# Kernel optimization log

Hardware: AMD Instinct MI355X
Metric: run time of the kernel (lower is better)

Reference implementation:

```python
import jax, jax.numpy as jnp
import numpy as np

B, T, V, Dw, Df, H, L, F_ = 16, 96, 32000, 512, 512, 1024, 100, 64
EPS = 1e-8
SOS = 0


def setup_inputs() -> dict:
    key = jax.random.key(0)
    ks = jax.random.split(key, 24)
    rn = lambda k, s, sc=0.02: (jax.random.normal(k, s) * sc).astype(jnp.float32)
    pos_mask = (jax.random.uniform(ks[1], (B, F_, L)) < 0.3).astype(jnp.float32)
    pos_mask = jnp.maximum(pos_mask, jax.nn.one_hot(jnp.zeros((B, F_), jnp.int32), L))
    return {
        "fact_embeddings": rn(ks[0], (B, F_, Df), 1.0),
        "pos_mask": pos_mask,
        "emb": rn(ks[2], (V, Dw), 0.05),
        "W_ih": rn(ks[3], (4 * H, Df + Dw + L)),
        "W_hh": rn(ks[4], (4 * H, H)),
        "b_ih": jnp.zeros(4 * H, jnp.float32),
        "b_hh": jnp.zeros(4 * H, jnp.float32),
        "Wf1": rn(ks[5], (H, H + Df)), "bf1": jnp.zeros(H, jnp.float32),
        "Wf2": rn(ks[6], (Df, H)), "bf2": jnp.zeros(Df, jnp.float32),
        "Wc1": rn(ks[7], (H, H + Df)), "bc1": jnp.zeros(H, jnp.float32),
        "Wc2": rn(ks[8], (1, H)), "bc2": jnp.zeros(1, jnp.float32),
        "Wv1": rn(ks[9], (H, H + Df)), "bv1": jnp.zeros(H, jnp.float32),
        "Wv2": rn(ks[10], (Dw, H)), "bv2": jnp.zeros(Dw, jnp.float32),
        "Wp1": rn(ks[11], (H, H + Df)), "bp1": jnp.zeros(H, jnp.float32),
        "Wp2": rn(ks[12], (100, H)), "bp2": jnp.zeros(100, jnp.float32),
        "WP": rn(ks[13], (L, 100)), "bP": jnp.zeros(L, jnp.float32),
        "true_w": jax.random.randint(ks[14], (B, T), 0, L),
        "true_a": jax.random.randint(ks[15], (B, T), 0, F_),
        "true_z": jax.random.randint(ks[16], (B, T), 0, 2),
        "num_facts": jax.random.randint(ks[17], (B,), 1, F_),
    }


def reference(fact_embeddings, pos_mask, emb, W_ih, W_hh, b_ih, b_hh,
              Wf1, bf1, Wf2, bf2, Wc1, bc1, Wc2, bc2,
              Wv1, bv1, Wv2, bv2, Wp1, bp1, Wp2, bp2, WP, bP,
              true_w, true_a, true_z, num_facts):
    def mlp(x, W1, b1, W2, b2):
        return W2 @ jax.nn.relu(W1 @ x + b1) + b2

    def single(fe, pmask_b, tw, ta, tz, nf):
        # fe: [F_, Df]  pmask_b: [F_, L]  tw/ta/tz: [T]
        idx = jnp.arange(F_)
        valid = (idx < nf).astype(jnp.float32)
        attn_mask = jnp.where(idx == F_ - 1, 1.0, valid)  # NaF slot always allowed
        e_k = (fe * valid[:, None]).sum(0) / nf.astype(jnp.float32)

        def step(carry, inputs):
            a_prev, h, c, wv, wo = carry
            w_t, a_true, z_true = inputs
            x = jnp.concatenate([a_prev, wv, wo])  # [Df+Dw+L]
            gates = W_ih @ x + b_ih + W_hh @ h + b_hh
            i_g, f_g, g_g, o_g = jnp.split(gates, 4)
            c = jax.nn.sigmoid(f_g) * c + jax.nn.sigmoid(i_g) * jnp.tanh(g_g)
            h = jax.nn.sigmoid(o_g) * jnp.tanh(c)
            oe = jnp.concatenate([h, e_k])
            k_fact = mlp(oe, Wf1, bf1, Wf2, bf2)           # [Df]
            prob_a = jax.nn.softmax(fe @ k_fact)           # [F_]
            m = attn_mask * prob_a + EPS
            m = m / m.sum()
            log_m = jnp.log(m)
            a_idx = jnp.argmax(m)
            a_vec = fe[a_idx]
            oa = jnp.concatenate([h, a_vec])
            z = jax.nn.sigmoid(mlp(oa, Wc1, bc1, Wc2, bc2))[0]
            k_voca = mlp(oa, Wv1, bv1, Wv2, bv2)           # [Dw]
            log_w = jax.nn.log_softmax(emb @ k_voca)       # [V]
            k_pos = mlp(oa, Wp1, bp1, Wp2, bp2)            # [100]
            prob_pos = jax.nn.softmax(WP @ k_pos + bP)     # [L]
            mp = pmask_b[a_true] * prob_pos + EPS
            mp = mp / mp.sum()
            log_pos = jnp.log(mp)
            zf = z_true.astype(jnp.float32)
            loss = (-log_m[a_true]
                    + jnp.where(z_true == 0, -log_w[w_t], -log_pos[w_t])
                    - (zf * jnp.log(z) + (1.0 - zf) * jnp.log(1.0 - z)))
            wv_next = jnp.where(z_true == 0, emb[w_t], jnp.zeros(Dw, jnp.float32))
            wo_next = jnp.where(z_true == 0, jnp.zeros(L, jnp.float32), jax.nn.one_hot(w_t, L))
            return (a_vec, h, c, wv_next, wo_next), loss

        carry0 = (jnp.zeros(Df, jnp.float32), jnp.zeros(H, jnp.float32),
                  jnp.zeros(H, jnp.float32), emb[SOS], jnp.zeros(L, jnp.float32))
        _, losses = jax.lax.scan(step, carry0, (tw, ta, tz))
        return losses.sum()

    return jax.vmap(single)(fact_embeddings, pos_mask, true_w, true_a, true_z, num_facts).sum()
```

## Files before the change

kernel.cpp:

```cpp
#include <hip/hip_runtime.h>
#include <math.h>

#define TT 96
#define VV 32000
#define EPSF 1e-8f

typedef __attribute__((ext_vector_type(8))) short short8;
typedef __attribute__((ext_vector_type(4))) float f4v;

__device__ __forceinline__ float wsum64(float v){
  #pragma unroll
  for (int m=32;m>0;m>>=1) v += __shfl_xor(v,m);
  return v;
}
__device__ __forceinline__ float sigm(float x){ return 1.0f/(1.0f+expf(-x)); }
__device__ __forceinline__ float softplus(float x){ return x>20.0f ? x : log1pf(expf(x)); }
__device__ __forceinline__ float bf2f(unsigned short u){ return __uint_as_float(((unsigned)u)<<16); }
__device__ __forceinline__ unsigned short f2bf(float f){
  unsigned u = __float_as_uint(f);
  return (unsigned short)((u + 0x7fffu + ((u>>16)&1u)) >> 16);
}

__device__ __forceinline__ void core_chunk(
  const float4* __restrict__ w0, const float4* __restrict__ w1,
  const float4* __restrict__ w2, const float4* __restrict__ w3,
  const float4* __restrict__ xl, int l, int g, float (&acc)[4][4])
{
  #pragma unroll
  for (int kt=0; kt<8; kt++){
    int i = kt*16 + l;
    float4 a0=w0[i], a1=w1[i], a2=w2[i], a3=w3[i];
    #pragma unroll
    for (int j=0;j<4;j++){
      float4 x = xl[(4*g+j)*129 + i];
      acc[0][j] += a0.x*x.x + a0.y*x.y + a0.z*x.z + a0.w*x.w;
      acc[1][j] += a1.x*x.x + a1.y*x.y + a1.z*x.z + a1.w*x.w;
      acc[2][j] += a2.x*x.x + a2.y*x.y + a2.z*x.z + a2.w*x.w;
      acc[3][j] += a3.x*x.x + a3.y*x.y + a3.z*x.z + a3.w*x.w;
    }
  }
}

__device__ __forceinline__ float reduce_pick(float (&acc)[4][4], int l){
  float r = 0.f;
  #pragma unroll
  for (int ri=0;ri<4;ri++)
  #pragma unroll
  for (int j=0;j<4;j++){
    float v = acc[ri][j];
    v += __shfl_xor(v,1); v += __shfl_xor(v,2);
    v += __shfl_xor(v,4); v += __shfl_xor(v,8);
    if (l == ri*4+j) r = v;
  }
  return r;
}


__global__ __launch_bounds__(256) void k_step1(
  const float* __restrict__ Whh, float* __restrict__ hall,
  const float* __restrict__ Pw, const float* __restrict__ Pa,
  const int* __restrict__ aall, float* __restrict__ c, int t)
{
  __shared__ float4 xl[16*129];
  __shared__ float sg[256];
  int tid = threadIdx.x, lane = tid & 63, wave = tid >> 6;
  int l = lane & 15, g = lane >> 4;
  int j0 = blockIdx.x*4;
  const float4* h4 = (const float4*)hall + (size_t)t*4096;
  float acc[4][4] = {};
  for (int kc=0; kc<2; kc++){
    for (int idx=tid; idx<2048; idx+=256){
      int b = idx>>7, i = idx&127;
      xl[b*129+i] = h4[b*256 + kc*128 + i];
    }
    __syncthreads();
    const float4* w0 = (const float4*)(Whh + (size_t)(wave*1024 + j0+0)*1024) + kc*128;
    const float4* w1 = (const float4*)(Whh + (size_t)(wave*1024 + j0+1)*1024) + kc*128;
    const float4* w2 = (const float4*)(Whh + (size_t)(wave*1024 + j0+2)*1024) + kc*128;
    const float4* w3 = (const float4*)(Whh + (size_t)(wave*1024 + j0+3)*1024) + kc*128;
    core_chunk(w0,w1,w2,w3, xl, l, g, acc);
    __syncthreads();
  }
  float v = reduce_pick(acc, l);
  int r = l>>2;
  int b = g*4 + (l&3);
  int row = wave*1024 + j0 + r;
  float e = Pw[((size_t)(b*96+t))*4096 + row];
  if (t > 0){
    int ai = aall[(t-1)*16 + b];
    e += Pa[((size_t)(b*64+ai))*4096 + row];
  }
  sg[wave*64 + r*16 + b] = v + e;
  __syncthreads();
  if (tid < 64){
    int jj = j0 + (tid>>4), bb = tid&15;
    float ig = sg[  0 + (tid>>4)*16 + bb];
    float fg = sg[ 64 + (tid>>4)*16 + bb];
    float gg = sg[128 + (tid>>4)*16 + bb];
    float og = sg[192 + (tid>>4)*16 + bb];
    int ci = bb*1024 + jj;
    float cn = sigm(fg)*c[ci] + sigm(ig)*tanhf(gg);
    c[ci] = cn;
    hall[((size_t)(t+1)*16 + bb)*1024 + jj] = sigm(og)*tanhf(cn);
  }
}

__global__ __launch_bounds__(256) void k_tf(
  const float* __restrict__ Wf1, const float* __restrict__ hall,
  const float* __restrict__ cf, float* __restrict__ tf, int t)
{
  __shared__ float4 xl[16*129];
  int tid = threadIdx.x, lane = tid & 63, wave = tid >> 6;
  int l = lane & 15, g = lane >> 4;
  int rl0 = blockIdx.x*16 + wave*4;
  const float4* h4 = (const float4*)hall + (size_t)(t+1)*4096;
  float acc[4][4] = {};
  for (int kc=0; kc<2; kc++){
    for (int idx=tid; idx<2048; idx+=256){
      int b = idx>>7, i = idx&127;
      xl[b*129+i] = h4[b*256 + kc*128 + i];
    }
    __syncthreads();
    const float4* w0 = (const float4*)(Wf1 + (size_t)(rl0+0)*1536) + kc*128;
    const float4* w1 = (const float4*)(Wf1 + (size_t)(rl0+1)*1536) + kc*128;
    const float4* w2 = (const float4*)(Wf1 + (size_t)(rl0+2)*1536) + kc*128;
    const float4* w3 = (const float4*)(Wf1 + (size_t)(rl0+3)*1536) + kc*128;
    core_chunk(w0,w1,w2,w3, xl, l, g, acc);
    __syncthreads();
  }
  float v = reduce_pick(acc, l);
  int rl = rl0 + (l>>2);
  int b = g*4 + (l&3);
  tf[b*1024 + rl] = fmaxf(v + cf[b*1024 + rl], 0.f);
}

__global__ __launch_bounds__(256) void k_fk(
  const float* __restrict__ Wf2, const float* __restrict__ bf2,
  const float* __restrict__ tf, float* __restrict__ kfact)
{
  __shared__ float4 xl[16*129];
  int tid = threadIdx.x, lane = tid & 63, wave = tid >> 6;
  int l = lane & 15, g = lane >> 4;
  int row0 = blockIdx.x*16 + wave*4;
  const float4* X4 = (const float4*)tf;
  float acc[4][4] = {};
  for (int kc=0; kc<2; kc++){
    for (int idx=tid; idx<2048; idx+=256){
      int b = idx>>7, i = idx&127;
      xl[b*129+i] = X4[b*256 + kc*128 + i];
    }
    __syncthreads();
    const float4* w0 = (const float4*)(Wf2 + (size_t)(row0+0)*1024) + kc*128;
    const float4* w1 = (const float4*)(Wf2 + (size_t)(row0+1)*1024) + kc*128;
    const float4* w2 = (const float4*)(Wf2 + (size_t)(row0+2)*1024) + kc*128;
    const float4* w3 = (const float4*)(Wf2 + (size_t)(row0+3)*1024) + kc*128;
    core_chunk(w0,w1,w2,w3, xl, l, g, acc);
    __syncthreads();
  }
  float v = reduce_pick(acc, l);
  int row = row0 + (l>>2);
  int b = g*4 + (l&3);
  kfact[b*512 + row] = v + bf2[row];
}

__global__ __launch_bounds__(256) void k_attn(
  const float* __restrict__ fe, const float* __restrict__ kfact,
  const int* __restrict__ ta, const int* __restrict__ nfp,
  int* __restrict__ aall, float* __restrict__ loss, int t)
{
  __shared__ float sS[64];
  int b = blockIdx.x, tid = threadIdx.x;
  int f = tid >> 2, q = tid & 3;
  const float4* fe4 = (const float4*)(fe + ((size_t)b*64 + f)*512);
  const float4* kf4 = (const float4*)(kfact + b*512);
  float acc = 0.f;
  for (int j=0;j<32;j++){
    int i = q*32 + j;
    float4 a = fe4[i], k = kf4[i];
    acc += a.x*k.x + a.y*k.y + a.z*k.z + a.w*k.w;
  }
  acc += __shfl_xor(acc,1);
  acc += __shfl_xor(acc,2);
  if (q==0) sS[f] = acc;
  __syncthreads();
  if (tid < 64){
    int nf = nfp[b];
    float s = sS[tid];
    float mx = s;
    #pragma unroll
    for (int m=32;m>0;m>>=1) mx = fmaxf(mx, __shfl_xor(mx,m));
    float p = expf(s - mx);
    float ps = wsum64(p);
    p /= ps;
    bool mask = (tid < nf) || (tid == 63);
    float mval = mask ? (p + EPSF) : EPSF;
    float msum = wsum64(mval);
    float bv = mval; int bi2 = tid;
    #pragma unroll
    for (int m=32;m>0;m>>=1){
      float ov = __shfl_xor(bv,m); int oi = __shfl_xor(bi2,m);
      if (ov > bv || (ov == bv && oi < bi2)){ bv = ov; bi2 = oi; }
    }
    int at = ta[b*TT + t];
    float mat = __shfl(mval, at);
    if (tid == 0){
      atomicAdd(loss, -(logf(mat) - logf(msum)));
      aall[t*16 + b] = bi2;
    }
  }
}


__global__ __launch_bounds__(256) void k2_cvp(
  const float* __restrict__ Wc1, const float* __restrict__ Wv1,
  const float* __restrict__ Wp1, const float* __restrict__ hall,
  const float* __restrict__ Ph, const int* __restrict__ aall,
  const float* __restrict__ bc1, const float* __restrict__ bv1,
  const float* __restrict__ bp1, float* __restrict__ tcvp)
{
  __shared__ float4 xl[16*129];
  int tid = threadIdx.x, lane = tid & 63, wave = tid >> 6;
  int l = lane & 15, g = lane >> 4;
  int seg = blockIdx.x >> 6;
  int rl0 = (blockIdx.x & 63)*16 + wave*4;
  const float* W = (seg==0)?Wc1:(seg==1)?Wv1:Wp1;
  const float4* h4 = (const float4*)hall + (size_t)(16 + blockIdx.y*16)*256;
  float acc[4][4] = {};
  for (int kc=0; kc<2; kc++){
    for (int idx=tid; idx<2048; idx+=256){
      int cc = idx>>7, i = idx&127;
      xl[cc*129+i] = h4[cc*256 + kc*128 + i];
    }
    __syncthreads();
    const float4* w0 = (const float4*)(W + (size_t)(rl0+0)*1536) + kc*128;
    const float4* w1 = (const float4*)(W + (size_t)(rl0+1)*1536) + kc*128;
    const float4* w2 = (const float4*)(W + (size_t)(rl0+2)*1536) + kc*128;
    const float4* w3 = (const float4*)(W + (size_t)(rl0+3)*1536) + kc*128;
    core_chunk(w0,w1,w2,w3, xl, l, g, acc);
    __syncthreads();
  }
  float v = reduce_pick(acc, l);
  int rl = rl0 + (l>>2);
  int n = blockIdx.y*16 + g*4 + (l&3);
  int b = n & 15;
  int ai = aall[n];
  const float* bias = (seg==0)?bc1:(seg==1)?bv1:bp1;
  float vv = v + Ph[((size_t)(b*64+ai))*3072 + seg*1024 + rl] + bias[rl];
  tcvp[(size_t)n*3072 + seg*1024 + rl] = fmaxf(vv, 0.f);
}

__global__ __launch_bounds__(256) void k2_heads2(
  const float* __restrict__ Wv2, const float* __restrict__ bv2,
  const float* __restrict__ Wp2, const float* __restrict__ bp2,
  const float* __restrict__ Wc2, const float* __restrict__ bc2,
  const float* __restrict__ tcvp, unsigned short* __restrict__ kvh,
  float* __restrict__ kpall, float* __restrict__ zlall)
{
  __shared__ float4 xl[16*129];
  int tid = threadIdx.x, lane = tid & 63, wave = tid >> 6;
  int l = lane & 15, g = lane >> 4;
  int bx = blockIdx.x;
  int seg = (bx < 32) ? 0 : (bx < 39) ? 1 : 2;
  int rb  = (seg==0) ? bx*16 : (seg==1) ? (bx-32)*16 : 0;
  int rl0 = rb + wave*4;
  const float* WS = (seg==0)?Wv2:(seg==1)?Wp2:Wc2;
  int maxr = (seg==0)?511:(seg==1)?99:0;
  int xoff4 = (seg==0)?256:(seg==1)?512:0;
  const float4* X4 = (const float4*)tcvp;
  float acc[4][4] = {};
  for (int kc=0; kc<2; kc++){
    for (int idx=tid; idx<2048; idx+=256){
      int cc = idx>>7, i = idx&127;
      xl[cc*129+i] = X4[(size_t)(blockIdx.y*16+cc)*768 + xoff4 + kc*128 + i];
    }
    __syncthreads();
    const float4* w0 = (const float4*)(WS + (size_t)min(rl0+0,maxr)*1024) + kc*128;
    const float4* w1 = (const float4*)(WS + (size_t)min(rl0+1,maxr)*1024) + kc*128;
    const float4* w2 = (const float4*)(WS + (size_t)min(rl0+2,maxr)*1024) + kc*128;
    const float4* w3 = (const float4*)(WS + (size_t)min(rl0+3,maxr)*1024) + kc*128;
    core_chunk(w0,w1,w2,w3, xl, l, g, acc);
    __syncthreads();
  }
  float v = reduce_pick(acc, l);
  int rl = rl0 + (l>>2);
  int n = blockIdx.y*16 + g*4 + (l&3);
  if (seg==0) kvh[(size_t)n*512 + rl] = f2bf(v + bv2[rl]);
  else if (seg==1){ if (rl < 100) kpall[n*128 + rl] = v + bp2[rl]; }
  else { if (rl == 0) zlall[n] = v + bc2[0]; }
}

__global__ __launch_bounds__(256) void k2_vocab(
  const unsigned short* __restrict__ embh, const unsigned short* __restrict__ kvh,
  float2* __restrict__ part)
{
  int wid = blockIdx.x*4 + (threadIdx.x>>6);
  int lane = threadIdx.x & 63;
  int mtile = wid % 500, ntile = wid / 500;
  int mrow = mtile*64 + (lane&15);
  int ncol = ntile*64 + (lane&15);
  int ko = (lane>>4)*8;
  f4v acc[4][4];
  #pragma unroll
  for (int i=0;i<4;i++)
  #pragma unroll
  for (int j=0;j<4;j++)
  #pragma unroll
  for (int r=0;r<4;r++) acc[i][j][r] = 0.f;
  for (int kk=0; kk<512; kk+=32){
    short8 af[4], bfr[4];
    #pragma unroll
    for (int i=0;i<4;i++)
      af[i] = *(const short8*)(embh + (size_t)(mrow+16*i)*512 + kk + ko);
    #pragma unroll
    for (int i=0;i<4;i++)
      bfr[i] = *(const short8*)(kvh + (size_t)(ncol+16*i)*512 + kk + ko);
    #pragma unroll
    for (int i=0;i<4;i++)
      #pragma unroll
      for (int j=0;j<4;j++)
        acc[i][j] = __builtin_amdgcn_mfma_f32_16x16x32_bf16(af[i], bfr[j], acc[i][j], 0,0,0);
  }
  int q = lane>>4;
  #pragma unroll
  for (int j=0;j<4;j++){
    float mx = -3.4e38f;
    #pragma unroll
    for (int i=0;i<4;i++)
    #pragma unroll
    for (int r=0;r<4;r++) mx = fmaxf(mx, acc[i][j][r]);
    mx = fmaxf(mx, __shfl_xor(mx,16));
    mx = fmaxf(mx, __shfl_xor(mx,32));
    float s = 0.f;
    #pragma unroll
    for (int i=0;i<4;i++)
    #pragma unroll
    for (int r=0;r<4;r++) s += expf(acc[i][j][r] - mx);
    s += __shfl_xor(s,16);
    s += __shfl_xor(s,32);
    if (q==0){
      int col = ntile*64 + 16*j + (lane&15);
      part[(size_t)col*500 + mtile] = make_float2(mx, s);
    }
  }
}

__global__ __launch_bounds__(256) void k2_vfin(
  const float2* __restrict__ part, const unsigned short* __restrict__ embh,
  const unsigned short* __restrict__ kvh, const int* __restrict__ tw,
  const int* __restrict__ tz, float* __restrict__ loss)
{
  __shared__ float red[4];
  int n = blockIdx.x, tid = threadIdx.x;
  int t = n>>4, b = n&15;
  float mx = -3.4e38f;
  for (int i=tid; i<500; i+=256) mx = fmaxf(mx, part[(size_t)n*500+i].x);
  #pragma unroll
  for (int m=32;m>0;m>>=1) mx = fmaxf(mx, __shfl_xor(mx,m));
  if ((tid&63)==0) red[tid>>6] = mx;
  __syncthreads();
  float M = fmaxf(fmaxf(red[0],red[1]), fmaxf(red[2],red[3]));
  __syncthreads();
  float s = 0.f;
  for (int i=tid; i<500; i+=256){
    float2 p = part[(size_t)n*500+i];
    s += p.y * expf(p.x - M);
  }
  s = wsum64(s);
  if ((tid&63)==0) red[tid>>6] = s;
  __syncthreads();
  float S = red[0]+red[1]+red[2]+red[3];
  __syncthreads();
  int w = tw[b*96+t];
  float d = 0.f;
  {
    const unsigned short* er = embh + (size_t)w*512;
    const unsigned short* kr = kvh + (size_t)n*512;
    for (int i=tid; i<512; i+=256) d += bf2f(er[i])*bf2f(kr[i]);
  }
  d = wsum64(d);
  if ((tid&63)==0) red[tid>>6] = d;
  __syncthreads();
  if (tid==0 && tz[b*96+t]==0){
    float D = red[0]+red[1]+red[2]+red[3];
    atomicAdd(loss, -(D - (M + logf(S))));
  }
}

__global__ __launch_bounds__(128) void k2_posz(
  const float* __restrict__ kpall, const float* __restrict__ zlall,
  const float* __restrict__ WP, const float* __restrict__ bP,
  const float* __restrict__ pmask, const int* __restrict__ tw,
  const int* __restrict__ ta, const int* __restrict__ tz,
  float* __restrict__ loss)
{
  __shared__ float pp[100];
  int n = blockIdx.x, tid = threadIdx.x;
  int t = n>>4, b = n&15;
  if (tid < 100){
    float s = bP[tid];
    const float* wr = WP + tid*100;
    const float* kp = kpall + n*128;
    for (int j=0;j<100;j++) s += wr[j]*kp[j];
    pp[tid] = s;
  }
  __syncthreads();
  if (tid == 0){
    float u = zlall[n];
    int z = tz[b*96+t], w = tw[b*96+t], at = ta[b*96+t];
    float tot = z ? softplus(-u) : softplus(u);
    if (z){
      float mxv = -1e30f;
      for (int l2=0;l2<100;l2++) mxv = fmaxf(mxv, pp[l2]);
      float se = 0.f;
      for (int l2=0;l2<100;l2++) se += expf(pp[l2]-mxv);
      const float* pm = pmask + ((size_t)b*64 + at)*100;
      float msum = 0.f, mw = 0.f;
      for (int l2=0;l2<100;l2++){
        float m = pm[l2]*(expf(pp[l2]-mxv)/se) + EPSF;
        msum += m;
        if (l2==w) mw = m;
      }
      tot += -(logf(mw) - logf(msum));
    }
    atomicAdd(loss, tot);
  }
}


__global__ void k_cvt_emb(const float* __restrict__ emb, unsigned* __restrict__ out){
  const int n = VV*512/2;
  for (int idx = blockIdx.x*256 + threadIdx.x; idx < n; idx += gridDim.x*256){
    float2 v = ((const float2*)emb)[idx];
    unsigned a = __float_as_uint(v.x), b = __float_as_uint(v.y);
    unsigned ra = (a + 0x7fffu + ((a>>16)&1u)) >> 16;
    unsigned rb = (b + 0x7fffu + ((b>>16)&1u)) >> 16;
    out[idx] = ra | (rb<<16);
  }
}

__global__ void k_setup(const float* __restrict__ fe, const int* __restrict__ nfp,
                        float* __restrict__ e_k){
  int b = blockIdx.x, tid = threadIdx.x;
  int nf = nfp[b];
  for (int d=tid; d<512; d+=256){
    float s = 0.f;
    for (int f=0; f<nf; f++) s += fe[((size_t)b*64+f)*512 + d];
    e_k[b*512+d] = s/(float)nf;
  }
}

__global__ __launch_bounds__(256) void k_pre_pa(
  const float* __restrict__ Wih, const float* __restrict__ fe, float* __restrict__ Pa)
{
  __shared__ float4 xl[16*129];
  int tid = threadIdx.x, lane = tid & 63, wave = tid >> 6;
  int l = lane & 15, g = lane >> 4;
  int row0 = blockIdx.x*16 + wave*4;
  int c0 = blockIdx.y*16;
  const float4* fe4 = (const float4*)fe;
  for (int idx=tid; idx<2048; idx+=256){
    int cc = idx>>7, i = idx&127;
    xl[cc*129+i] = fe4[(size_t)(c0+cc)*128 + i];
  }
  __syncthreads();
  const float4* w0 = (const float4*)(Wih + (size_t)(row0+0)*1124);
  const float4* w1 = (const float4*)(Wih + (size_t)(row0+1)*1124);
  const float4* w2 = (const float4*)(Wih + (size_t)(row0+2)*1124);
  const float4* w3 = (const float4*)(Wih + (size_t)(row0+3)*1124);
  float acc[4][4] = {};
  core_chunk(w0,w1,w2,w3, xl, l, g, acc);
  float v = reduce_pick(acc, l);
  int row = row0 + (l>>2), c = c0 + g*4 + (l&3);
  Pa[(size_t)c*4096 + row] = v;
}

__global__ __launch_bounds__(256) void k_pre_ph(
  const float* __restrict__ Wc1, const float* __restrict__ Wv1,
  const float* __restrict__ Wp1, const float* __restrict__ fe, float* __restrict__ Ph)
{
  __shared__ float4 xl[16*129];
  int tid = threadIdx.x, lane = tid & 63, wave = tid >> 6;
  int l = lane & 15, g = lane >> 4;
  int row0 = blockIdx.x*16 + wave*4;
  int head = row0 >> 10, rl0 = row0 & 1023;
  const float* W = (head==0)?Wc1:(head==1)?Wv1:Wp1;
  int c0 = blockIdx.y*16;
  const float4* fe4 = (const float4*)fe;
  for (int idx=tid; idx<2048; idx+=256){
    int cc = idx>>7, i = idx&127;
    xl[cc*129+i] = fe4[(size_t)(c0+cc)*128 + i];
  }
  __syncthreads();
  const float4* w0 = (const float4*)(W + (size_t)(rl0+0)*1536 + 1024);
  const float4* w1 = (const float4*)(W + (size_t)(rl0+1)*1536 + 1024);
  const float4* w2 = (const float4*)(W + (size_t)(rl0+2)*1536 + 1024);
  const float4* w3 = (const float4*)(W + (size_t)(rl0+3)*1536 + 1024);
  float acc[4][4] = {};
  core_chunk(w0,w1,w2,w3, xl, l, g, acc);
  float v = reduce_pick(acc, l);
  int row = row0 + (l>>2), c = c0 + g*4 + (l&3);
  Ph[(size_t)c*3072 + row] = v;
}

__global__ __launch_bounds__(256) void k_pre_pw(
  const float* __restrict__ Wih, const float* __restrict__ emb,
  const int* __restrict__ tw, const int* __restrict__ tz,
  const float* __restrict__ bih, const float* __restrict__ bhh,
  float* __restrict__ Pw)
{
  __shared__ float4 xl[16*129];
  int tid = threadIdx.x, lane = tid & 63, wave = tid >> 6;
  int l = lane & 15, g = lane >> 4;
  int row0 = blockIdx.x*16 + wave*4;
  int c0 = blockIdx.y*16;
  for (int idx=tid; idx<2048; idx+=256){
    int cc = idx>>7, i = idx&127;
    int c = c0+cc, b = c/96, t2 = c - b*96;
    int w=0, z=0;
    if (t2>0){ w = tw[b*96+t2-1]; z = tz[b*96+t2-1]; }
    float4 v = make_float4(0.f,0.f,0.f,0.f);
    if (z==0) v = ((const float4*)emb)[(size_t)w*128 + i];
    xl[cc*129+i] = v;
  }
  __syncthreads();
  const float4* w0 = (const float4*)(Wih + (size_t)(row0+0)*1124 + 512);
  const float4* w1 = (const float4*)(Wih + (size_t)(row0+1)*1124 + 512);
  const float4* w2 = (const float4*)(Wih + (size_t)(row0+2)*1124 + 512);
  const float4* w3 = (const float4*)(Wih + (size_t)(row0+3)*1124 + 512);
  float acc[4][4] = {};
  core_chunk(w0,w1,w2,w3, xl, l, g, acc);
  float v = reduce_pick(acc, l);
  int row = row0 + (l>>2), c = c0 + g*4 + (l&3);
  int b = c/96, t2 = c - b*96;
  int w=0, z=0;
  if (t2>0){ w = tw[b*96+t2-1]; z = tz[b*96+t2-1]; }
  v += bih[row] + bhh[row];
  if (z) v += Wih[(size_t)row*1124 + 1024 + w];
  Pw[(size_t)c*4096 + row] = v;
}

__global__ __launch_bounds__(256) void k_pre_cf(
  const float* __restrict__ Wf1, const float* __restrict__ bf1,
  const float* __restrict__ e_k, float* __restrict__ cf)
{
  __shared__ float4 xl[16*129];
  int tid = threadIdx.x, lane = tid & 63, wave = tid >> 6;
  int l = lane & 15, g = lane >> 4;
  int row0 = blockIdx.x*16 + wave*4;
  const float4* ek4 = (const float4*)e_k;
  for (int idx=tid; idx<2048; idx+=256){
    int cc = idx>>7, i = idx&127;
    xl[cc*129+i] = ek4[cc*128 + i];
  }
  __syncthreads();
  const float4* w0 = (const float4*)(Wf1 + (size_t)(row0+0)*1536 + 1024);
  const float4* w1 = (const float4*)(Wf1 + (size_t)(row0+1)*1536 + 1024);
  const float4* w2 = (const float4*)(Wf1 + (size_t)(row0+2)*1536 + 1024);
  const float4* w3 = (const float4*)(Wf1 + (size_t)(row0+3)*1536 + 1024);
  float acc[4][4] = {};
  core_chunk(w0,w1,w2,w3, xl, l, g, acc);
  float v = reduce_pick(acc, l);
  int row = row0 + (l>>2), b = g*4 + (l&3);
  cf[b*1024 + row] = v + bf1[row];
}

__global__ void k_out(const float* __restrict__ loss, float* __restrict__ out){
  out[0] = loss[0];
}

extern "C" void kernel_launch(void* const* d_in, const int* in_sizes, int n_in,
                              void* d_out, int out_size, void* d_ws, size_t ws_size,
                              hipStream_t stream)
{
  const float* fe   = (const float*)d_in[0];
  const float* pmask= (const float*)d_in[1];
  const float* emb  = (const float*)d_in[2];
  const float* Wih  = (const float*)d_in[3];
  const float* Whh  = (const float*)d_in[4];
  const float* bih  = (const float*)d_in[5];
  const float* bhh  = (const float*)d_in[6];
  const float* Wf1  = (const float*)d_in[7];
  const float* bf1  = (const float*)d_in[8];
  const float* Wf2  = (const float*)d_in[9];
  const float* bf2  = (const float*)d_in[10];
  const float* Wc1  = (const float*)d_in[11];
  const float* bc1  = (const float*)d_in[12];
  const float* Wc2  = (const float*)d_in[13];
  const float* bc2  = (const float*)d_in[14];
  const float* Wv1  = (const float*)d_in[15];
  const float* bv1  = (const float*)d_in[16];
  const float* Wv2  = (const float*)d_in[17];
  const float* bv2  = (const float*)d_in[18];
  const float* Wp1  = (const float*)d_in[19];
  const float* bp1  = (const float*)d_in[20];
  const float* Wp2  = (const float*)d_in[21];
  const float* bp2  = (const float*)d_in[22];
  const float* WP   = (const float*)d_in[23];
  const float* bP   = (const float*)d_in[24];
  const int* tw  = (const int*)d_in[25];
  const int* ta  = (const int*)d_in[26];
  const int* tz  = (const int*)d_in[27];
  const int* nfp = (const int*)d_in[28];

  float* w = (float*)d_ws;
  float*    loss  = w + 0;
  float*    c     = w + 16;
  float*    hall  = w + 16400;
  int*      aall  = (int*)(w + 1605648);
  float*    tf    = w + 1607184;
  float*    kfact = w + 1623568;
  float*    e_k   = w + 1631760;
  float*    cf    = w + 1639952;
  float*    kpall = w + 1656336;
  float*    zlall = w + 1852944;
  float*    tcvp  = w + 1854480;
  float2*   part  = (float2*)(w + 6573072);
  unsigned short* kvh = (unsigned short*)(w + 8109072);
  float*    Pa    = w + 8502288;
  float*    Ph    = w + 12696592;
  float*    Pw    = w + 15842320;
  unsigned* embbf = (unsigned*)(w + 22133776);
  const unsigned short* embh = (const unsigned short*)embbf;

  hipMemsetAsync(d_ws, 0, (size_t)(16 + 16384 + 16384)*4, stream);
  k_cvt_emb<<<8192,256,0,stream>>>(emb, embbf);
  k_setup<<<16,256,0,stream>>>(fe, nfp, e_k);
  k_pre_pa<<<dim3(256,64),256,0,stream>>>(Wih, fe, Pa);
  k_pre_ph<<<dim3(192,64),256,0,stream>>>(Wc1, Wv1, Wp1, fe, Ph);
  k_pre_pw<<<dim3(256,96),256,0,stream>>>(Wih, emb, tw, tz, bih, bhh, Pw);
  k_pre_cf<<<64,256,0,stream>>>(Wf1, bf1, e_k, cf);

  for (int t=0; t<TT; t++){
    k_step1<<<256,256,0,stream>>>(Whh, hall, Pw, Pa, aall, c, t);
    k_tf<<<64,256,0,stream>>>(Wf1, hall, cf, tf, t);
    k_fk<<<32,256,0,stream>>>(Wf2, bf2, tf, kfact);
    k_attn<<<16,256,0,stream>>>(fe, kfact, ta, nfp, aall, loss, t);
  }

  k2_cvp<<<dim3(192,96),256,0,stream>>>(Wc1, Wv1, Wp1, hall, Ph, aall,
                                        bc1, bv1, bp1, tcvp);
  k2_heads2<<<dim3(40,96),256,0,stream>>>(Wv2, bv2, Wp2, bp2, Wc2, bc2,
                                          tcvp, kvh, kpall, zlall);
  k2_vocab<<<3000,256,0,stream>>>(embh, kvh, part);
  k2_vfin<<<1536,256,0,stream>>>(part, embh, kvh, tw, tz, loss);
  k2_posz<<<1536,128,0,stream>>>(kpall, zlall, WP, bP, pmask, tw, ta, tz, loss);
  k_out<<<1,1,0,stream>>>(loss, (float*)d_out);
}
```

Baseline: 5.384 ms.

## Fuse recurrent timestep loop into one persistent kernel with grid barriers

Replaces the 96×4 per-timestep kernel launches with a single persistent 256-block kernel that steps through time using atomic grid-wide barriers. It also folds Wf2 into the attention scores by precomputing E = fe·Wf2 and C0 = fe·bf2, which removes the kfact GEMV stage. The LSTM gate nonlinearity moves into 16 per-batch blocks that read gate pre-activations from a global buffer. This removes launch overhead and one dependent stage per step. In exchange, correctness depends on all 256 blocks being co-resident, the barrier counter relies on zeroed workspace, and the gate update now runs on few blocks.

```diff
diff --git a/kernel.cpp b/kernel.cpp
--- a/kernel.cpp
+++ b/kernel.cpp
@@ -56,157 +56,148 @@
 }
 
 
-__global__ __launch_bounds__(256) void k_step1(
-  const float* __restrict__ Whh, float* __restrict__ hall,
+__device__ __forceinline__ float tile16(
+  const float* __restrict__ W, int row0, int ldw,
+  const float4* __restrict__ xl, int l, int g)
+{
+  const float4* w0 = (const float4*)(W + (size_t)(row0+0)*ldw);
+  const float4* w1 = (const float4*)(W + (size_t)(row0+1)*ldw);
+  const float4* w2 = (const float4*)(W + (size_t)(row0+2)*ldw);
+  const float4* w3 = (const float4*)(W + (size_t)(row0+3)*ldw);
+  float acc[4][4] = {};
+  #pragma unroll
+  for (int kt=0; kt<16; kt++){
+    int i = kt*16 + l;
+    float4 a0=w0[i], a1=w1[i], a2=w2[i], a3=w3[i];
+    #pragma unroll
+    for (int j=0;j<4;j++){
+      float4 x = xl[(4*g+j)*257 + i];
+      acc[0][j] += a0.x*x.x + a0.y*x.y + a0.z*x.z + a0.w*x.w;
+      acc[1][j] += a1.x*x.x + a1.y*x.y + a1.z*x.z + a1.w*x.w;
+      acc[2][j] += a2.x*x.x + a2.y*x.y + a2.z*x.z + a2.w*x.w;
+      acc[3][j] += a3.x*x.x + a3.y*x.y + a3.z*x.z + a3.w*x.w;
+    }
+  }
+  return reduce_pick(acc, l);
+}
+
+__device__ __forceinline__ void gbar(unsigned* bar, int rnd){
+  __syncthreads();
+  if (threadIdx.x == 0){
+    __threadfence();
+    __hip_atomic_fetch_add(bar, 1u, __ATOMIC_ACQ_REL, __HIP_MEMORY_SCOPE_AGENT);
+    unsigned target = (unsigned)(rnd+1)*256u;
+    while (__hip_atomic_load(bar, __ATOMIC_ACQUIRE, __HIP_MEMORY_SCOPE_AGENT) < target)
+      __builtin_amdgcn_s_sleep(2);
+  }
+  __syncthreads();
+}
+
+__global__ __launch_bounds__(256) void k_seq(
+  const float* __restrict__ Whh, const float* __restrict__ Wf1,
   const float* __restrict__ Pw, const float* __restrict__ Pa,
-  const int* __restrict__ aall, float* __restrict__ c, int t)
-{
-  __shared__ float4 xl[16*129];
-  __shared__ float sg[256];
-  int tid = threadIdx.x, lane = tid & 63, wave = tid >> 6;
-  int l = lane & 15, g = lane >> 4;
-  int j0 = blockIdx.x*4;
-  const float4* h4 = (const float4*)hall + (size_t)t*4096;
-  float acc[4][4] = {};
-  for (int kc=0; kc<2; kc++){
-    for (int idx=tid; idx<2048; idx+=256){
-      int b = idx>>7, i = idx&127;
-      xl[b*129+i] = h4[b*256 + kc*128 + i];
-    }
-    __syncthreads();
-    const float4* w0 = (const float4*)(Whh + (size_t)(wave*1024 + j0+0)*1024) + kc*128;
-    const float4* w1 = (const float4*)(Whh + (size_t)(wave*1024 + j0+1)*1024) + kc*128;
-    const float4* w2 = (const float4*)(Whh + (size_t)(wave*1024 + j0+2)*1024) + kc*128;
-    const float4* w3 = (const float4*)(Whh + (size_t)(wave*1024 + j0+3)*1024) + kc*128;
-    core_chunk(w0,w1,w2,w3, xl, l, g, acc);
-    __syncthreads();
-  }
-  float v = reduce_pick(acc, l);
-  int r = l>>2;
-  int b = g*4 + (l&3);
-  int row = wave*1024 + j0 + r;
-  float e = Pw[((size_t)(b*96+t))*4096 + row];
-  if (t > 0){
-    int ai = aall[(t-1)*16 + b];
-    e += Pa[((size_t)(b*64+ai))*4096 + row];
-  }
-  sg[wave*64 + r*16 + b] = v + e;
-  __syncthreads();
-  if (tid < 64){
-    int jj = j0 + (tid>>4), bb = tid&15;
-    float ig = sg[  0 + (tid>>4)*16 + bb];
-    float fg = sg[ 64 + (tid>>4)*16 + bb];
-    float gg = sg[128 + (tid>>4)*16 + bb];
-    float og = sg[192 + (tid>>4)*16 + bb];
-    int ci = bb*1024 + jj;
-    float cn = sigm(fg)*c[ci] + sigm(ig)*tanhf(gg);
-    c[ci] = cn;
-    hall[((size_t)(t+1)*16 + bb)*1024 + jj] = sigm(og)*tanhf(cn);
-  }
-}
-
-__global__ __launch_bounds__(256) void k_tf(
-  const float* __restrict__ Wf1, const float* __restrict__ hall,
-  const float* __restrict__ cf, float* __restrict__ tf, int t)
-{
-  __shared__ float4 xl[16*129];
-  int tid = threadIdx.x, lane = tid & 63, wave = tid >> 6;
-  int l = lane & 15, g = lane >> 4;
-  int rl0 = blockIdx.x*16 + wave*4;
-  const float4* h4 = (const float4*)hall + (size_t)(t+1)*4096;
-  float acc[4][4] = {};
-  for (int kc=0; kc<2; kc++){
-    for (int idx=tid; idx<2048; idx+=256){
-      int b = idx>>7, i = idx&127;
-      xl[b*129+i] = h4[b*256 + kc*128 + i];
-    }
-    __syncthreads();
-    const float4* w0 = (const float4*)(Wf1 + (size_t)(rl0+0)*1536) + kc*128;
-    const float4* w1 = (const float4*)(Wf1 + (size_t)(rl0+1)*1536) + kc*128;
-    const float4* w2 = (const float4*)(Wf1 + (size_t)(rl0+2)*1536) + kc*128;
-    const float4* w3 = (const float4*)(Wf1 + (size_t)(rl0+3)*1536) + kc*128;
-    core_chunk(w0,w1,w2,w3, xl, l, g, acc);
-    __syncthreads();
-  }
-  float v = reduce_pick(acc, l);
-  int rl = rl0 + (l>>2);
-  int b = g*4 + (l&3);
-  tf[b*1024 + rl] = fmaxf(v + cf[b*1024 + rl], 0.f);
-}
-
-__global__ __launch_bounds__(256) void k_fk(
-  const float* __restrict__ Wf2, const float* __restrict__ bf2,
-  const float* __restrict__ tf, float* __restrict__ kfact)
-{
-  __shared__ float4 xl[16*129];
-  int tid = threadIdx.x, lane = tid & 63, wave = tid >> 6;
-  int l = lane & 15, g = lane >> 4;
-  int row0 = blockIdx.x*16 + wave*4;
-  const float4* X4 = (const float4*)tf;
-  float acc[4][4] = {};
-  for (int kc=0; kc<2; kc++){
-    for (int idx=tid; idx<2048; idx+=256){
-      int b = idx>>7, i = idx&127;
-      xl[b*129+i] = X4[b*256 + kc*128 + i];
-    }
-    __syncthreads();
-    const float4* w0 = (const float4*)(Wf2 + (size_t)(row0+0)*1024) + kc*128;
-    const float4* w1 = (const float4*)(Wf2 + (size_t)(row0+1)*1024) + kc*128;
-    const float4* w2 = (const float4*)(Wf2 + (size_t)(row0+2)*1024) + kc*128;
-    const float4* w3 = (const float4*)(Wf2 + (size_t)(row0+3)*1024) + kc*128;
-    core_chunk(w0,w1,w2,w3, xl, l, g, acc);
-    __syncthreads();
-  }
-  float v = reduce_pick(acc, l);
-  int row = row0 + (l>>2);
-  int b = g*4 + (l&3);
-  kfact[b*512 + row] = v + bf2[row];
-}
-
-__global__ __launch_bounds__(256) void k_attn(
-  const float* __restrict__ fe, const float* __restrict__ kfact,
-  const int* __restrict__ ta, const int* __restrict__ nfp,
-  int* __restrict__ aall, float* __restrict__ loss, int t)
-{
+  const float* __restrict__ cf, const float* __restrict__ E,
+  const float* __restrict__ C0, const int* __restrict__ ta,
+  const int* __restrict__ nfp,
+  float* __restrict__ hall, float* __restrict__ c, float* __restrict__ tf,
+  float* __restrict__ Gw, int* __restrict__ aall,
+  float* __restrict__ loss, unsigned* __restrict__ bar)
+{
+  __shared__ float4 xl[16*257];
   __shared__ float sS[64];
-  int b = blockIdx.x, tid = threadIdx.x;
-  int f = tid >> 2, q = tid & 3;
-  const float4* fe4 = (const float4*)(fe + ((size_t)b*64 + f)*512);
-  const float4* kf4 = (const float4*)(kfact + b*512);
-  float acc = 0.f;
-  for (int j=0;j<32;j++){
-    int i = q*32 + j;
-    float4 a = fe4[i], k = kf4[i];
-    acc += a.x*k.x + a.y*k.y + a.z*k.z + a.w*k.w;
-  }
-  acc += __shfl_xor(acc,1);
-  acc += __shfl_xor(acc,2);
-  if (q==0) sS[f] = acc;
-  __syncthreads();
-  if (tid < 64){
-    int nf = nfp[b];
-    float s = sS[tid];
-    float mx = s;
-    #pragma unroll
-    for (int m=32;m>0;m>>=1) mx = fmaxf(mx, __shfl_xor(mx,m));
-    float p = expf(s - mx);
-    float ps = wsum64(p);
-    p /= ps;
-    bool mask = (tid < nf) || (tid == 63);
-    float mval = mask ? (p + EPSF) : EPSF;
-    float msum = wsum64(mval);
-    float bv = mval; int bi2 = tid;
-    #pragma unroll
-    for (int m=32;m>0;m>>=1){
-      float ov = __shfl_xor(bv,m); int oi = __shfl_xor(bi2,m);
-      if (ov > bv || (ov == bv && oi < bi2)){ bv = ov; bi2 = oi; }
-    }
-    int at = ta[b*TT + t];
-    float mat = __shfl(mval, at);
-    if (tid == 0){
-      atomicAdd(loss, -(logf(mat) - logf(msum)));
-      aall[t*16 + b] = bi2;
-    }
+  __shared__ int sIdx;
+  int tid = threadIdx.x, bx = blockIdx.x;
+  int lane = tid & 63, wave = tid >> 6, l = lane & 15, g = lane >> 4;
+
+  for (int i = 0; i <= 96; i++){
+    {
+      const float4* h4 = (const float4*)hall + (size_t)i*4096;
+      for (int idx=tid; idx<4096; idx+=256){
+        int b2 = idx>>8, ii = idx&255;
+        xl[b2*257+ii] = h4[b2*256+ii];
+      }
+      __syncthreads();
+      {
+        float v = tile16(Whh, bx*16 + wave*4, 1024, xl, l, g);
+        int row = bx*16 + wave*4 + (l>>2);
+        int b = g*4 + (l&3);
+        Gw[b*4096 + row] = v;
+      }
+      if (bx < 64){
+        float v = tile16(Wf1, bx*16 + wave*4, 1536, xl, l, g);
+        int rw = bx*16 + wave*4 + (l>>2);
+        int b = g*4 + (l&3);
+        tf[b*1024 + rw] = fmaxf(v + cf[b*1024 + rw], 0.f);
+      }
+    }
+    gbar(bar, 2*i);
+
+    if (bx < 16){
+      int b = bx;
+      float* tfl = (float*)xl;
+      for (int j=tid; j<1024; j+=256) tfl[j] = tf[b*1024 + j];
+      __syncthreads();
+      int ai = 0;
+      if (i >= 1){
+        int f = tid>>2, q = tid&3;
+        const float4* Er = (const float4*)(E + (size_t)(b*64+f)*1024) + q*64;
+        const float4* tf4 = (const float4*)tfl + q*64;
+        float s_ = 0.f;
+        #pragma unroll 4
+        for (int k2=0;k2<64;k2++){
+          float4 e = Er[k2], x = tf4[k2];
+          s_ += e.x*x.x + e.y*x.y + e.z*x.z + e.w*x.w;
+        }
+        s_ += __shfl_xor(s_,1); s_ += __shfl_xor(s_,2);
+        if (q==0) sS[f] = s_ + C0[b*64+f];
+        __syncthreads();
+        if (tid < 64){
+          int nf = nfp[b];
+          float s = sS[tid];
+          float mx = s;
+          #pragma unroll
+          for (int m=32;m>0;m>>=1) mx = fmaxf(mx, __shfl_xor(mx,m));
+          float p = expf(s - mx);
+          float ps = wsum64(p);
+          p /= ps;
+          bool mask = (tid < nf) || (tid == 63);
+          float mval = mask ? (p + EPSF) : EPSF;
+          float msum = wsum64(mval);
+          float bv = mval; int bi2 = tid;
+          #pragma unroll
+          for (int m=32;m>0;m>>=1){
+            float ov = __shfl_xor(bv,m); int oi = __shfl_xor(bi2,m);
+            if (ov > bv || (ov == bv && oi < bi2)){ bv = ov; bi2 = oi; }
+          }
+          int at = ta[b*TT + (i-1)];
+          float mat = __shfl(mval, at);
+          if (tid == 0){
+            atomicAdd(loss, -(logf(mat) - logf(msum)));
+            sIdx = bi2;
+          }
+        }
+        __syncthreads();
+        ai = sIdx;
+        if (tid == 0) aall[(i-1)*16 + b] = ai;
+      }
+      if (i <= 95){
+        const float* gb = Gw + b*4096;
+        const float* pw = Pw + (size_t)(b*96 + i)*4096;
+        const float* pa = Pa + (size_t)(b*64 + ai)*4096;
+        bool hasA = (i >= 1);
+        for (int j=tid; j<1024; j+=256){
+          float ig = gb[j]        + pw[j]        + (hasA ? pa[j]        : 0.f);
+          float fg = gb[1024+j]   + pw[1024+j]   + (hasA ? pa[1024+j]   : 0.f);
+          float gg = gb[2048+j]   + pw[2048+j]   + (hasA ? pa[2048+j]   : 0.f);
+          float og = gb[3072+j]   + pw[3072+j]   + (hasA ? pa[3072+j]   : 0.f);
+          float co = c[b*1024 + j];
+          float cn = sigm(fg)*co + sigm(ig)*tanhf(gg);
+          c[b*1024 + j] = cn;
+          hall[((size_t)(i+1)*16 + b)*1024 + j] = sigm(og)*tanhf(cn);
+        }
+      }
+    }
+    gbar(bar, 2*i+1);
   }
 }
 
@@ -562,6 +553,41 @@
   float v = reduce_pick(acc, l);
   int row = row0 + (l>>2), b = g*4 + (l&3);
   cf[b*1024 + row] = v + bf1[row];
+}
+
+__global__ __launch_bounds__(256) void k_pre_e(
+  const float* __restrict__ fe, const float* __restrict__ Wf2, float* __restrict__ E)
+{
+  __shared__ float fel[16*512];
+  int tid = threadIdx.x;
+  int c0 = blockIdx.x*16;
+  int j0 = blockIdx.y*256;
+  const float4* fe4 = (const float4*)fe;
+  for (int idx=tid; idx<2048; idx+=256)
+    ((float4*)fel)[idx] = fe4[(size_t)c0*128 + idx];
+  __syncthreads();
+  int j = j0 + tid;
+  float acc[16] = {};
+  for (int d=0; d<512; d++){
+    float wv = Wf2[d*1024 + j];
+    #pragma unroll
+    for (int cc=0; cc<16; cc++) acc[cc] += fel[cc*512+d]*wv;
+  }
+  #pragma unroll
+  for (int cc=0; cc<16; cc++) E[(size_t)(c0+cc)*1024 + j] = acc[cc];
+}
+
+__global__ void k_pre_c0(const float* __restrict__ fe, const float* __restrict__ bf2,
+                         float* __restrict__ C0)
+{
+  int b = blockIdx.x, tid = threadIdx.x;
+  int f = tid>>2, q = tid&3;
+  const float4* fr = (const float4*)(fe + (size_t)(b*64+f)*512) + q*32;
+  const float4* b4 = (const float4*)bf2 + q*32;
+  float s = 0.f;
+  for (int k=0;k<32;k++){ float4 a=fr[k], w=b4[k]; s += a.x*w.x+a.y*w.y+a.z*w.z+a.w*w.w; }
+  s += __shfl_xor(s,1); s += __shfl_xor(s,2);
+  if (q==0) C0[b*64+f] = s;
 }
 
 __global__ void k_out(const float* __restrict__ loss, float* __restrict__ out){
@@ -604,22 +630,25 @@
 
   float* w = (float*)d_ws;
   float*    loss  = w + 0;
+  unsigned* bar   = (unsigned*)(w + 8);
   float*    c     = w + 16;
   float*    hall  = w + 16400;
   int*      aall  = (int*)(w + 1605648);
   float*    tf    = w + 1607184;
-  float*    kfact = w + 1623568;
-  float*    e_k   = w + 1631760;
-  float*    cf    = w + 1639952;
-  float*    kpall = w + 1656336;
-  float*    zlall = w + 1852944;
-  float*    tcvp  = w + 1854480;
-  float2*   part  = (float2*)(w + 6573072);
-  unsigned short* kvh = (unsigned short*)(w + 8109072);
-  float*    Pa    = w + 8502288;
-  float*    Ph    = w + 12696592;
-  float*    Pw    = w + 15842320;
-  unsigned* embbf = (unsigned*)(w + 22133776);
+  float*    Gw    = w + 1623568;
+  float*    e_k   = w + 1689104;
+  float*    cf    = w + 1697296;
+  float*    E     = w + 1713680;
+  float*    C0    = w + 2762256;
+  float*    kpall = w + 2763280;
+  float*    zlall = w + 2959888;
+  float*    tcvp  = w + 2961424;
+  float2*   part  = (float2*)(w + 7680016);
+  unsigned short* kvh = (unsigned short*)(w + 9216016);
+  float*    Pa    = w + 9609232;
+  float*    Ph    = w + 13803536;
+  float*    Pw    = w + 16949264;
+  unsigned* embbf = (unsigned*)(w + 23240720);
   const unsigned short* embh = (const unsigned short*)embbf;
 
   hipMemsetAsync(d_ws, 0, (size_t)(16 + 16384 + 16384)*4, stream);
@@ -629,13 +658,11 @@
   k_pre_ph<<<dim3(192,64),256,0,stream>>>(Wc1, Wv1, Wp1, fe, Ph);
   k_pre_pw<<<dim3(256,96),256,0,stream>>>(Wih, emb, tw, tz, bih, bhh, Pw);
   k_pre_cf<<<64,256,0,stream>>>(Wf1, bf1, e_k, cf);
-
-  for (int t=0; t<TT; t++){
-    k_step1<<<256,256,0,stream>>>(Whh, hall, Pw, Pa, aall, c, t);
-    k_tf<<<64,256,0,stream>>>(Wf1, hall, cf, tf, t);
-    k_fk<<<32,256,0,stream>>>(Wf2, bf2, tf, kfact);
-    k_attn<<<16,256,0,stream>>>(fe, kfact, ta, nfp, aall, loss, t);
-  }
+  k_pre_e<<<dim3(64,4),256,0,stream>>>(fe, Wf2, E);
+  k_pre_c0<<<16,256,0,stream>>>(fe, bf2, C0);
+
+  k_seq<<<256,256,0,stream>>>(Whh, Wf1, Pw, Pa, cf, E, C0, ta, nfp,
+                              hall, c, tf, Gw, aall, loss, bar);
 
   k2_cvp<<<dim3(192,96),256,0,stream>>>(Wc1, Wv1, Wp1, hall, Ph, aall,
                                         bc1, bv1, bp1, tcvp);
```

After: 16.89 ms. +213.7%, slower.
